# Kernel tuning notes

Hardware: AMD Instinct MI355X
Metric: run time of the kernel (lower is better)

The kernel has to match this reference:

```python
import jax, jax.numpy as jnp
import numpy as np

COL = 0
K = 5  # n_neighbors
BIG = 1e10  # torch.nan_to_num replacement used before topk


def setup_inputs() -> dict:
    key = jax.random.key(0)
    k1, k2, k3, k4, k5 = jax.random.split(key, 5)
    Nq, Nt, D = 4096, 16384, 32
    X = jax.random.normal(k1, (Nq, D), jnp.float32)
    # strictly positive distances (no exact zeros / NaNs)
    dist_chunk = jax.random.uniform(k2, (Nq, Nt), jnp.float32) + 1e-3
    _fit_X = jax.random.normal(k3, (Nt, D), jnp.float32)
    mask_fit_X = jax.random.uniform(k4, (Nt, D)) < 0.1          # missing mask of fit data
    non_missing_fix_X = ~mask_fit_X                              # consistent, as in KNNImputer
    mask = jax.random.uniform(k5, (Nq, D)) < 0.2                 # missing mask of X
    dist_idx_map = jnp.arange(Nq, dtype=jnp.int32)
    row_missing_idx = jnp.arange(Nq, dtype=jnp.int32)
    return {"X": X, "dist_chunk": dist_chunk, "non_missing_fix_X": non_missing_fix_X,
            "mask_fit_X": mask_fit_X, "dist_idx_map": dist_idx_map, "mask": mask,
            "row_missing_idx": row_missing_idx, "_fit_X": _fit_X}


def _impute_column(X, dist_chunk, non_missing_fix_X, mask_fit_X,
                   dist_idx_map, mask, row_missing_idx, _fit_X):
    col = COL
    Nq = X.shape[0]
    potential = non_missing_fix_X[:, col]                        # [Nt] bool: valid donors
    # receivers = rows listed in row_missing_idx whose col is missing (static-shape mask)
    in_missing = jnp.zeros((Nq,), bool).at[row_missing_idx].set(True)
    receiver = in_missing & mask[:, col]                         # [Nq]

    d = dist_chunk[dist_idx_map]                                 # [Nq, Nt]
    d_pot = jnp.where(potential[None, :], d, jnp.inf)

    # rows where every potential-donor distance is NaN -> column-mean fallback
    has_valid = jnp.any(potential[None, :] & ~jnp.isnan(d), axis=1)
    all_nan = ~has_valid

    # topk smallest with NaN -> 1e10 (SubTopKIndices)
    dn = jnp.where(jnp.isnan(d_pot), BIG, d_pot)
    _, donors_idx = jax.lax.top_k(-dn, K)                        # [Nq, K] smallest dists
    donors_dist = jnp.take_along_axis(d_pot, donors_idx, axis=1) # keeps NaNs like original

    # weights == 'distance' (_get_weights) then NaN -> 0 (SubWeightMatrix)
    w = 1.0 / donors_dist
    inf_mask = jnp.isinf(w)
    inf_row = jnp.any(inf_mask, axis=1)
    w = jnp.where(inf_row[:, None], inf_mask.astype(w.dtype), w)
    w = jnp.where(jnp.isnan(w), 0.0, w)

    donors = _fit_X[donors_idx, col]                             # [Nq, K]
    donors_mask = 1.0 - mask_fit_X[donors_idx, col].astype(w.dtype)
    valid = potential[donors_idx].astype(w.dtype)                # guard (inf donors weight 0)
    new_w = donors_mask * w * valid                              # MakeNewWeights
    ws = jnp.sum(new_w, axis=1)
    div = jnp.where(ws == 0, 1.0, ws)
    knn_val = jnp.sum(donors * new_w, axis=1) / div              # [Nq]

    # column mean over observed fit values (all-NaN fallback)
    obs = (~mask_fit_X[:, col]).astype(X.dtype)
    msum = jnp.sum(obs)
    csum = jnp.sum(obs * _fit_X[:, col])
    col_mean = csum / jnp.where(msum > 0, msum, 1.0)

    new_col = jnp.where(receiver, jnp.where(all_nan, col_mean, knn_val), X[:, col])
    return X.at[:, col].set(new_col)


def reference(X, dist_chunk, non_missing_fix_X, mask_fit_X,
              dist_idx_map, mask, row_missing_idx, _fit_X):
    return _impute_column(X, dist_chunk, non_missing_fix_X, mask_fit_X,
                          dist_idx_map, mask, row_missing_idx, _fit_X)
```

## Files before the change

kernel.cpp:

```cpp
#include <hip/hip_runtime.h>
#include <math.h>

#define NQ 4096
#define NT 16384
#define DD 32
#define COLIDX 0
#define BIGF 1.0e10f
#define INFF __builtin_inff()

typedef unsigned long long u64;

#define ROW_VECS (NT / 4)
#define ROWS_PER_BLOCK 2
#define P1_BLOCKS (NQ / ROWS_PER_BLOCK)

#define SENT_BITS 0x7F800000FFFFFFFFULL

__device__ __forceinline__ int boolat(const void* p, long long idx, int w32) {
    if (w32) return ((const int*)p)[idx] != 0;
    return ((const unsigned char*)p)[idx] != 0;
}

__device__ __forceinline__ int detect_w32(const void* nm, const void* mk,
                                          int tid, int* s_bad) {
    if (tid == 0) *s_bad = 0;
    __syncthreads();
    const unsigned char* nm8 = (const unsigned char*)nm;
    const unsigned char* mk8 = (const unsigned char*)mk;
    int bad = 0;
    for (int b = tid; b < 4096; b += 256)
        if ((int)nm8[b] + (int)mk8[b] != 1) bad = 1;
    if (bad) atomicOr(s_bad, 1);
    __syncthreads();
    return *s_bad ? 1 : 0;
}

__global__ __launch_bounds__(256) void prep1_kernel(
    const void* __restrict__ nm, const void* __restrict__ mk,
    const float* __restrict__ fitX,
    int* __restrict__ wflag, float* __restrict__ partial,
    unsigned char* __restrict__ inmiss, unsigned char* __restrict__ pot8)
{
    __shared__ int s_bad;
    __shared__ float sc[256], sm[256];
    const int tid = threadIdx.x;
    const int w32 = detect_w32(nm, mk, tid, &s_bad);
    if (blockIdx.x == 0 && tid == 0) *wflag = w32;

    const int t = blockIdx.x * 256 + tid;
    pot8[t] = (unsigned char)boolat(nm, (long long)t * DD + COLIDX, w32);

    float cs = 0.0f, ms = 0.0f;
    if (!boolat(mk, (long long)t * DD + COLIDX, w32)) {
        cs = fitX[(long long)t * DD + COLIDX];
        ms = 1.0f;
    }
    sc[tid] = cs; sm[tid] = ms;
    __syncthreads();
#pragma unroll
    for (int s = 128; s > 0; s >>= 1) {
        if (tid < s) { sc[tid] += sc[tid + s]; sm[tid] += sm[tid + s]; }
        __syncthreads();
    }
    if (tid == 0) { partial[blockIdx.x * 2] = sc[0]; partial[blockIdx.x * 2 + 1] = sm[0]; }

    if (t < NQ) inmiss[t] = 0;
}

__global__ __launch_bounds__(256) void prep2_kernel(
    const int* __restrict__ rmi, const float* __restrict__ partial,
    float* __restrict__ cmean, unsigned char* __restrict__ inmiss)
{
    const int tid = threadIdx.x;
    for (int i = tid; i < NQ; i += 256) {
        int r = rmi[i];
        if (r >= 0 && r < NQ) inmiss[r] = 1;
    }
    if (tid < 64) {
        float c = partial[2 * tid];
        float m = partial[2 * tid + 1];
#pragma unroll
        for (int off = 32; off >= 1; off >>= 1) {
            c += __shfl_down(c, off, 64);
            m += __shfl_down(m, off, 64);
        }
        if (tid == 0) *cmean = c / (m > 0.0f ? m : 1.0f);
    }
}

__device__ __forceinline__ double mkkeyd(float d, unsigned char p, unsigned idx) {
    const float key = (p != 0) ? fminf(d, BIGF) : INFF;
    const u64 bits = ((u64)__float_as_uint(key) << 32) | (u64)idx;
    return __longlong_as_double((long long)bits);
}

__device__ __forceinline__ void casd(double& x, double& y) {
    const double lo = fmin(x, y);
    const double hi = fmax(x, y);
    x = lo; y = hi;
}

__device__ __forceinline__ void merge5d(double a[5], const double b[5]) {
    double m0 = fmin(a[0], b[4]);
    double m1 = fmin(a[1], b[3]);
    double m2 = fmin(a[2], b[2]);
    double m3 = fmin(a[3], b[1]);
    double m4 = fmin(a[4], b[0]);
    casd(m0, m4);
    casd(m1, m3); casd(m2, m4);
    casd(m1, m2); casd(m3, m4);
    a[0] = m0; a[1] = m1; a[2] = m2; a[3] = m3; a[4] = m4;
}

__global__ __launch_bounds__(256, 8) void pass1_kernel(
    const float* __restrict__ dist,
    const unsigned char* __restrict__ pot8,
    u64* __restrict__ wslists)
{
    __shared__ double sv[3][5];
    const int tid = threadIdx.x;
    const uchar4* pvec = (const uchar4*)pot8;
    const double SENT = __longlong_as_double((long long)SENT_BITS);

#pragma unroll 1
    for (int rr = 0; rr < ROWS_PER_BLOCK; ++rr) {
        const int row = blockIdx.x * ROWS_PER_BLOCK + rr;
        const float4* dvec = (const float4*)dist + (long long)row * ROW_VECS;

        double v[5];
#pragma unroll
        for (int k = 0; k < 5; ++k) v[k] = SENT;

#pragma unroll 1
        for (int half = 0; half < 4; ++half) {
            float4 dd[4]; uchar4 pp[4];
#pragma unroll
            for (int g = 0; g < 4; ++g) {
                const int vi = (half * 4 + g) * 256 + tid;
                dd[g] = dvec[vi];
                pp[g] = pvec[vi];
            }
#pragma unroll
            for (int g = 0; g < 4; ++g) {
                const unsigned base =
                    (unsigned)(((half * 4 + g) * 256 + tid) * 4);
                double s0 = mkkeyd(dd[g].x, pp[g].x, base + 0);
                double s1 = mkkeyd(dd[g].y, pp[g].y, base + 1);
                double s2 = mkkeyd(dd[g].z, pp[g].z, base + 2);
                double s3 = mkkeyd(dd[g].w, pp[g].w, base + 3);
                const double gmin = fmin(fmin(s0, s1), fmin(s2, s3));
                if (__any(gmin < v[4])) {
                    casd(s0, s1); casd(s2, s3);
                    casd(s0, s2); casd(s1, s3);
                    casd(s1, s2);
                    double m0 = v[0];
                    double m1 = fmin(v[1], s3);
                    double m2 = fmin(v[2], s2);
                    double m3 = fmin(v[3], s1);
                    double m4 = fmin(v[4], s0);
                    casd(m0, m4);
                    casd(m1, m3); casd(m2, m4);
                    casd(m1, m2); casd(m3, m4);
                    v[0] = m0; v[1] = m1; v[2] = m2; v[3] = m3; v[4] = m4;
                }
            }
        }

#pragma unroll
        for (int mask = 1; mask <= 32; mask <<= 1) {
            double b[5];
#pragma unroll
            for (int k = 0; k < 5; ++k) b[k] = __shfl_xor(v[k], mask, 64);
            merge5d(v, b);
        }

        const int wave = tid >> 6;
        if (wave > 0 && (tid & 63) == 0) {
#pragma unroll
            for (int k = 0; k < 5; ++k) sv[wave - 1][k] = v[k];
        }
        __syncthreads();
        if (tid == 0) {
            double b[5];
#pragma unroll
            for (int w = 0; w < 3; ++w) {
                b[0] = sv[w][0]; b[1] = sv[w][1]; b[2] = sv[w][2];
                b[3] = sv[w][3]; b[4] = sv[w][4];
                merge5d(v, b);
            }
#pragma unroll
            for (int k = 0; k < 5; ++k)
                wslists[(long long)row * 5 + k] =
                    (u64)__double_as_longlong(v[k]);
        }
        __syncthreads();
    }
}

__global__ __launch_bounds__(256) void pass2_kernel(
    const float* __restrict__ X,
    const u64* __restrict__ wslists,
    const void* __restrict__ maskp,
    const void* __restrict__ mkfitp,
    const float* __restrict__ fitX,
    const int* __restrict__ dmap,
    const int* __restrict__ wflagp,
    const float* __restrict__ cmeanp,
    const unsigned char* __restrict__ inmiss,
    const unsigned char* __restrict__ pot8,
    float* __restrict__ out)
{
    const int gid = blockIdx.x * 256 + threadIdx.x;
    if (gid >= NQ * DD / 4) return;
    float4 v4 = ((const float4*)X)[gid];

    if ((gid & 7) == 0) {
        const int r = gid >> 3;
        const int q = dmap[r];
        u64 v[5];
        const u64* lp = wslists + (long long)q * 5;
#pragma unroll
        for (int i = 0; i < 5; ++i) v[i] = lp[i];

        const int w32 = *wflagp;
        const bool has_valid = (unsigned)(v[0] >> 32) < __float_as_uint(BIGF);
        const bool receiver =
            inmiss[r] && boolat(maskp, (long long)r * DD + COLIDX, w32);

        float val;
        if (!receiver) {
            val = v4.x;
        } else if (!has_valid) {
            val = *cmeanp;
        } else {
            float keyf[5]; bool ok[5]; int idxc[5];
#pragma unroll
            for (int i = 0; i < 5; ++i) {
                keyf[i] = __uint_as_float((unsigned)(v[i] >> 32));
                const unsigned id = (unsigned)(v[i] & 0xFFFFFFFFu);
                ok[i] = id < NT;
                idxc[i] = ok[i] ? (int)id : 0;
            }
            float dnr[5]; int mfv[5]; unsigned char vldb[5];
#pragma unroll
            for (int i = 0; i < 5; ++i)
                dnr[i] = fitX[(long long)idxc[i] * DD + COLIDX];
#pragma unroll
            for (int i = 0; i < 5; ++i)
                mfv[i] = boolat(mkfitp, (long long)idxc[i] * DD + COLIDX, w32);
#pragma unroll
            for (int i = 0; i < 5; ++i) vldb[i] = pot8[idxc[i]];

            float wk[5];
            bool infrow = false;
#pragma unroll
            for (int i = 0; i < 5; ++i) {
                const float dpot = (keyf[i] == BIGF) ? __builtin_nanf("") : keyf[i];
                const float t = 1.0f / dpot;
                wk[i] = ok[i] ? t : 0.0f;
                if (ok[i] && isinf(t)) infrow = true;
            }
            if (infrow) {
#pragma unroll
                for (int i = 0; i < 5; ++i) wk[i] = isinf(wk[i]) ? 1.0f : 0.0f;
            }
#pragma unroll
            for (int i = 0; i < 5; ++i) if (wk[i] != wk[i]) wk[i] = 0.0f;

            float wsum = 0.0f, vsum = 0.0f;
#pragma unroll
            for (int i = 0; i < 5; ++i) {
                const float dm = ok[i] ? (1.0f - (float)mfv[i]) : 0.0f;
                const float vl = ok[i] ? (float)vldb[i] : 0.0f;
                const float nw = dm * wk[i] * vl;
                wsum += nw;
                vsum += dnr[i] * nw;
            }
            const float div = (wsum == 0.0f) ? 1.0f : wsum;
            val = vsum / div;
        }
        v4.x = val;
    }
    ((float4*)out)[gid] = v4;
}

extern "C" void kernel_launch(void* const* d_in, const int* in_sizes, int n_in,
                              void* d_out, int out_size, void* d_ws, size_t ws_size,
                              hipStream_t stream) {
    const float* X     = (const float*)d_in[0];
    const float* dist  = (const float*)d_in[1];
    const void*  nm    = d_in[2];
    const void*  mkfit = d_in[3];
    const int*   dmap  = (const int*)d_in[4];
    const void*  maskp = d_in[5];
    const int*   rmi   = (const int*)d_in[6];
    const float* fitX  = (const float*)d_in[7];
    float* out = (float*)d_out;

    u64*   wslists = (u64*)d_ws;
    char*  base    = (char*)d_ws + (size_t)NQ * 5 * 8;
    int*   wflag   = (int*)base;
    float* cmean   = (float*)(base + 4);
    float* partial = (float*)(base + 8);
    unsigned char* inmiss = (unsigned char*)base + 520;
    unsigned char* pot8   = (unsigned char*)base + 520 + NQ;

    prep1_kernel<<<64, 256, 0, stream>>>(nm, mkfit, fitX, wflag, partial,
                                         inmiss, pot8);
    prep2_kernel<<<1, 256, 0, stream>>>(rmi, partial, cmean, inmiss);
    pass1_kernel<<<P1_BLOCKS, 256, 0, stream>>>(dist, pot8, wslists);
    pass2_kernel<<<(NQ * DD / 4 + 255) / 256, 256, 0, stream>>>(
        X, wslists, maskp, mkfit, fitX, dmap, wflag, cmean, inmiss, pot8, out);
}
```

Before: 68.14 us.

## Fold prep2 into pass1, copy X in prep1, drop topk early-skip branch

```diff
diff --git a/kernel.cpp b/kernel.cpp
--- a/kernel.cpp
+++ b/kernel.cpp
@@ -37,9 +37,10 @@
 
 __global__ __launch_bounds__(256) void prep1_kernel(
     const void* __restrict__ nm, const void* __restrict__ mk,
-    const float* __restrict__ fitX,
+    const float* __restrict__ fitX, const float* __restrict__ X,
     int* __restrict__ wflag, float* __restrict__ partial,
-    unsigned char* __restrict__ inmiss, unsigned char* __restrict__ pot8)
+    unsigned char* __restrict__ inmiss, unsigned char* __restrict__ pot8,
+    float* __restrict__ out)
 {
     __shared__ int s_bad;
     __shared__ float sc[256], sm[256];
@@ -65,27 +66,11 @@
     if (tid == 0) { partial[blockIdx.x * 2] = sc[0]; partial[blockIdx.x * 2 + 1] = sm[0]; }
 
     if (t < NQ) inmiss[t] = 0;
-}
-
-__global__ __launch_bounds__(256) void prep2_kernel(
-    const int* __restrict__ rmi, const float* __restrict__ partial,
-    float* __restrict__ cmean, unsigned char* __restrict__ inmiss)
-{
-    const int tid = threadIdx.x;
-    for (int i = tid; i < NQ; i += 256) {
-        int r = rmi[i];
-        if (r >= 0 && r < NQ) inmiss[r] = 1;
-    }
-    if (tid < 64) {
-        float c = partial[2 * tid];
-        float m = partial[2 * tid + 1];
-#pragma unroll
-        for (int off = 32; off >= 1; off >>= 1) {
-            c += __shfl_down(c, off, 64);
-            m += __shfl_down(m, off, 64);
-        }
-        if (tid == 0) *cmean = c / (m > 0.0f ? m : 1.0f);
-    }
+
+    const float4* Xv = (const float4*)X;
+    float4* outv = (float4*)out;
+    for (int i = t; i < NQ * DD / 4; i += 64 * 256)
+        outv[i] = Xv[i];
 }
 
 __device__ __forceinline__ double mkkeyd(float d, unsigned char p, unsigned idx) {
@@ -115,12 +100,33 @@
 __global__ __launch_bounds__(256, 8) void pass1_kernel(
     const float* __restrict__ dist,
     const unsigned char* __restrict__ pot8,
+    const int* __restrict__ rmi,
+    const float* __restrict__ partial,
+    float* __restrict__ cmean,
+    unsigned char* __restrict__ inmiss,
     u64* __restrict__ wslists)
 {
     __shared__ double sv[3][5];
     const int tid = threadIdx.x;
     const uchar4* pvec = (const uchar4*)pot8;
     const double SENT = __longlong_as_double((long long)SENT_BITS);
+
+    if (blockIdx.x == 0) {
+        for (int i = tid; i < NQ; i += 256) {
+            int r = rmi[i];
+            if (r >= 0 && r < NQ) inmiss[r] = 1;
+        }
+        if (tid < 64) {
+            float c = partial[2 * tid];
+            float m = partial[2 * tid + 1];
+#pragma unroll
+            for (int off = 32; off >= 1; off >>= 1) {
+                c += __shfl_down(c, off, 64);
+                m += __shfl_down(m, off, 64);
+            }
+            if (tid == 0) *cmean = c / (m > 0.0f ? m : 1.0f);
+        }
+    }
 
 #pragma unroll 1
     for (int rr = 0; rr < ROWS_PER_BLOCK; ++rr) {
@@ -148,21 +154,18 @@
                 double s1 = mkkeyd(dd[g].y, pp[g].y, base + 1);
                 double s2 = mkkeyd(dd[g].z, pp[g].z, base + 2);
                 double s3 = mkkeyd(dd[g].w, pp[g].w, base + 3);
-                const double gmin = fmin(fmin(s0, s1), fmin(s2, s3));
-                if (__any(gmin < v[4])) {
-                    casd(s0, s1); casd(s2, s3);
-                    casd(s0, s2); casd(s1, s3);
-                    casd(s1, s2);
-                    double m0 = v[0];
-                    double m1 = fmin(v[1], s3);
-                    double m2 = fmin(v[2], s2);
-                    double m3 = fmin(v[3], s1);
-                    double m4 = fmin(v[4], s0);
-                    casd(m0, m4);
-                    casd(m1, m3); casd(m2, m4);
-                    casd(m1, m2); casd(m3, m4);
-                    v[0] = m0; v[1] = m1; v[2] = m2; v[3] = m3; v[4] = m4;
-                }
+                casd(s0, s1); casd(s2, s3);
+                casd(s0, s2); casd(s1, s3);
+                casd(s1, s2);
+                double m0 = v[0];
+                double m1 = fmin(v[1], s3);
+                double m2 = fmin(v[2], s2);
+                double m3 = fmin(v[3], s1);
+                double m4 = fmin(v[4], s0);
+                casd(m0, m4);
+                casd(m1, m3); casd(m2, m4);
+                casd(m1, m2); casd(m3, m4);
+                v[0] = m0; v[1] = m1; v[2] = m2; v[3] = m3; v[4] = m4;
             }
         }
 
@@ -210,78 +213,73 @@
     const unsigned char* __restrict__ pot8,
     float* __restrict__ out)
 {
-    const int gid = blockIdx.x * 256 + threadIdx.x;
-    if (gid >= NQ * DD / 4) return;
-    float4 v4 = ((const float4*)X)[gid];
-
-    if ((gid & 7) == 0) {
-        const int r = gid >> 3;
-        const int q = dmap[r];
-        u64 v[5];
-        const u64* lp = wslists + (long long)q * 5;
-#pragma unroll
-        for (int i = 0; i < 5; ++i) v[i] = lp[i];
-
-        const int w32 = *wflagp;
-        const bool has_valid = (unsigned)(v[0] >> 32) < __float_as_uint(BIGF);
-        const bool receiver =
-            inmiss[r] && boolat(maskp, (long long)r * DD + COLIDX, w32);
-
-        float val;
-        if (!receiver) {
-            val = v4.x;
-        } else if (!has_valid) {
-            val = *cmeanp;
-        } else {
-            float keyf[5]; bool ok[5]; int idxc[5];
-#pragma unroll
-            for (int i = 0; i < 5; ++i) {
-                keyf[i] = __uint_as_float((unsigned)(v[i] >> 32));
-                const unsigned id = (unsigned)(v[i] & 0xFFFFFFFFu);
-                ok[i] = id < NT;
-                idxc[i] = ok[i] ? (int)id : 0;
-            }
-            float dnr[5]; int mfv[5]; unsigned char vldb[5];
-#pragma unroll
-            for (int i = 0; i < 5; ++i)
-                dnr[i] = fitX[(long long)idxc[i] * DD + COLIDX];
-#pragma unroll
-            for (int i = 0; i < 5; ++i)
-                mfv[i] = boolat(mkfitp, (long long)idxc[i] * DD + COLIDX, w32);
-#pragma unroll
-            for (int i = 0; i < 5; ++i) vldb[i] = pot8[idxc[i]];
-
-            float wk[5];
-            bool infrow = false;
-#pragma unroll
-            for (int i = 0; i < 5; ++i) {
-                const float dpot = (keyf[i] == BIGF) ? __builtin_nanf("") : keyf[i];
-                const float t = 1.0f / dpot;
-                wk[i] = ok[i] ? t : 0.0f;
-                if (ok[i] && isinf(t)) infrow = true;
-            }
-            if (infrow) {
-#pragma unroll
-                for (int i = 0; i < 5; ++i) wk[i] = isinf(wk[i]) ? 1.0f : 0.0f;
-            }
-#pragma unroll
-            for (int i = 0; i < 5; ++i) if (wk[i] != wk[i]) wk[i] = 0.0f;
-
-            float wsum = 0.0f, vsum = 0.0f;
-#pragma unroll
-            for (int i = 0; i < 5; ++i) {
-                const float dm = ok[i] ? (1.0f - (float)mfv[i]) : 0.0f;
-                const float vl = ok[i] ? (float)vldb[i] : 0.0f;
-                const float nw = dm * wk[i] * vl;
-                wsum += nw;
-                vsum += dnr[i] * nw;
-            }
-            const float div = (wsum == 0.0f) ? 1.0f : wsum;
-            val = vsum / div;
-        }
-        v4.x = val;
-    }
-    ((float4*)out)[gid] = v4;
+    const int r = blockIdx.x * 256 + threadIdx.x;
+    if (r >= NQ) return;
+
+    const int q = dmap[r];
+    u64 v[5];
+    const u64* lp = wslists + (long long)q * 5;
+#pragma unroll
+    for (int i = 0; i < 5; ++i) v[i] = lp[i];
+
+    const int w32 = *wflagp;
+    const bool has_valid = (unsigned)(v[0] >> 32) < __float_as_uint(BIGF);
+    const bool receiver =
+        inmiss[r] && boolat(maskp, (long long)r * DD + COLIDX, w32);
+
+    float val;
+    if (!receiver) {
+        val = X[(long long)r * DD + COLIDX];
+    } else if (!has_valid) {
+        val = *cmeanp;
+    } else {
+        float keyf[5]; bool ok[5]; int idxc[5];
+#pragma unroll
+        for (int i = 0; i < 5; ++i) {
+            keyf[i] = __uint_as_float((unsigned)(v[i] >> 32));
+            const unsigned id = (unsigned)(v[i] & 0xFFFFFFFFu);
+            ok[i] = id < NT;
+            idxc[i] = ok[i] ? (int)id : 0;
+        }
+        float dnr[5]; int mfv[5]; unsigned char vldb[5];
+#pragma unroll
+        for (int i = 0; i < 5; ++i)
+            dnr[i] = fitX[(long long)idxc[i] * DD + COLIDX];
+#pragma unroll
+        for (int i = 0; i < 5; ++i)
+            mfv[i] = boolat(mkfitp, (long long)idxc[i] * DD + COLIDX, w32);
+#pragma unroll
+        for (int i = 0; i < 5; ++i) vldb[i] = pot8[idxc[i]];
+
+        float wk[5];
+        bool infrow = false;
+#pragma unroll
+        for (int i = 0; i < 5; ++i) {
+            const float dpot = (keyf[i] == BIGF) ? __builtin_nanf("") : keyf[i];
+            const float t = 1.0f / dpot;
+            wk[i] = ok[i] ? t : 0.0f;
+            if (ok[i] && isinf(t)) infrow = true;
+        }
+        if (infrow) {
+#pragma unroll
+            for (int i = 0; i < 5; ++i) wk[i] = isinf(wk[i]) ? 1.0f : 0.0f;
+        }
+#pragma unroll
+        for (int i = 0; i < 5; ++i) if (wk[i] != wk[i]) wk[i] = 0.0f;
+
+        float wsum = 0.0f, vsum = 0.0f;
+#pragma unroll
+        for (int i = 0; i < 5; ++i) {
+            const float dm = ok[i] ? (1.0f - (float)mfv[i]) : 0.0f;
+            const float vl = ok[i] ? (float)vldb[i] : 0.0f;
+            const float nw = dm * wk[i] * vl;
+            wsum += nw;
+            vsum += dnr[i] * nw;
+        }
+        const float div = (wsum == 0.0f) ? 1.0f : wsum;
+        val = vsum / div;
+    }
+    out[(long long)r * DD + COLIDX] = val;
 }
 
 extern "C" void kernel_launch(void* const* d_in, const int* in_sizes, int n_in,
@@ -305,10 +303,10 @@
     unsigned char* inmiss = (unsigned char*)base + 520;
     unsigned char* pot8   = (unsigned char*)base + 520 + NQ;
 
-    prep1_kernel<<<64, 256, 0, stream>>>(nm, mkfit, fitX, wflag, partial,
-                                         inmiss, pot8);
-    prep2_kernel<<<1, 256, 0, stream>>>(rmi, partial, cmean, inmiss);
-    pass1_kernel<<<P1_BLOCKS, 256, 0, stream>>>(dist, pot8, wslists);
-    pass2_kernel<<<(NQ * DD / 4 + 255) / 256, 256, 0, stream>>>(
+    prep1_kernel<<<64, 256, 0, stream>>>(nm, mkfit, fitX, X, wflag, partial,
+                                         inmiss, pot8, out);
+    pass1_kernel<<<P1_BLOCKS, 256, 0, stream>>>(dist, pot8, rmi, partial,
+                                                cmean, inmiss, wslists);
+    pass2_kernel<<<(NQ + 255) / 256, 256, 0, stream>>>(
         X, wslists, maskp, mkfit, fitX, dmap, wflag, cmean, inmiss, pot8, out);
 }
```

Result: faster. 63.39 us (-7.0%).
